# Kernel tuning notes

Measured on AMD Instinct MI355X. Metric: run time of the kernel, lower is better.

## Reference

```python
import jax, jax.numpy as jnp
import numpy as np

EPS = 1e-12  # torch F.normalize default eps (clamp_min)

def _l2norm(v, axis):
    n = jnp.sqrt(jnp.sum(v * v, axis=axis, keepdims=True))
    return v / jnp.maximum(n, EPS)

def setup_inputs() -> dict:
    key = jax.random.key(0)
    k1, k2, k3 = jax.random.split(key, 3)
    N, D, H, W, K = 64, 128, 64, 64, 32
    x = jax.random.normal(k1, (N, D, H, W), dtype=jnp.float32)
    conv_w = jax.random.normal(k2, (K, D), dtype=jnp.float32)  # 1x1 conv weight, no bias
    centroids = jax.random.uniform(k3, (K, D), dtype=jnp.float32)
    return {"x": x, "conv_w": conv_w, "centroids": centroids}

def reference(x, conv_w, centroids):
    N, D, H, W = x.shape
    K = conv_w.shape[0]
    # descriptor-wise L2 normalization over channel dim
    x = _l2norm(x, axis=1)
    xf = x.reshape(N, D, H * W)                      # [N, D, P]
    # 1x1 conv == per-pixel linear: [K,D] @ [N,D,P] -> [N,K,P]
    logits = jnp.einsum('kd,ndp->nkp', conv_w, xf)
    soft_assign = jax.nn.softmax(logits, axis=1)     # softmax over clusters
    # vlad[n,k,d] = sum_p a[n,k,p]*(x[n,d,p] - c[k,d])
    #            = (a @ x^T)[n,k,d] - (sum_p a)[n,k] * c[k,d]
    agg = jnp.einsum('nkp,ndp->nkd', soft_assign, xf)
    asum = jnp.sum(soft_assign, axis=2)              # [N, K]
    vlad = agg - asum[:, :, None] * centroids[None]  # [N, K, D]
    vlad = _l2norm(vlad, axis=2)                     # intra-normalization
    vlad = vlad.reshape(N, K * D)
    vlad = _l2norm(vlad, axis=1)                     # global L2 norm
    return vlad
```

## Files before the change

kernel.cpp:

```cpp
#include <hip/hip_runtime.h>
#include <math.h>

#define N_IMG 64
#define D_CH  128
#define P_PIX 4096
#define K_CL  32
#define S_SPL 8
#define P_BLK (P_PIX / S_SPL)
#define TP    32
#define N_TILE (P_BLK / TP)

typedef __attribute__((ext_vector_type(8))) short bf16x8;
typedef __attribute__((ext_vector_type(4))) float f32x4;

#define MFMA(a, b, c) __builtin_amdgcn_mfma_f32_16x16x32_bf16(a, b, c, 0, 0, 0)

#define BAR() do {                                            \
    asm volatile("s_waitcnt lgkmcnt(0)" ::: "memory");        \
    __builtin_amdgcn_s_barrier();                             \
} while (0)

static __device__ __forceinline__ void split4t(float a, float b, float c, float d,
                                               ushort4 &h, ushort4 &l) {
    unsigned ua = __float_as_uint(a), ub = __float_as_uint(b);
    unsigned uc = __float_as_uint(c), ud = __float_as_uint(d);
    h.x = (ushort)(ua >> 16); h.y = (ushort)(ub >> 16);
    h.z = (ushort)(uc >> 16); h.w = (ushort)(ud >> 16);
    float ra = a - __uint_as_float(ua & 0xffff0000u);
    float rb = b - __uint_as_float(ub & 0xffff0000u);
    float rc = c - __uint_as_float(uc & 0xffff0000u);
    float rd = d - __uint_as_float(ud & 0xffff0000u);
    l.x = (ushort)(__float_as_uint(ra) >> 16);
    l.y = (ushort)(__float_as_uint(rb) >> 16);
    l.z = (ushort)(__float_as_uint(rc) >> 16);
    l.w = (ushort)(__float_as_uint(rd) >> 16);
}

#define STAGE_AND_PREFETCH(tt) do {                                          \
    const int cc_ = (tt) & 1;                                                \
    _Pragma("unroll")                                                        \
    for (int it = 0; it < 4; ++it) {                                         \
        int d_ = it * 32 + (tid >> 3);                                       \
        ushort4 h_, lo_;                                                     \
        split4t(xv[it].x, xv[it].y, xv[it].z, xv[it].w, h_, lo_);            \
        *(ushort4*)&xDh[cc_][d_ * 40 + 4 * (tid & 7)] = h_;                  \
        *(ushort4*)&xDl[cc_][d_ * 40 + 4 * (tid & 7)] = lo_;                 \
    }                                                                        \
    float sq_ = 0.f;                                                         \
    _Pragma("unroll")                                                        \
    for (int c_ = 0; c_ < 4; ++c_) {                                         \
        ushort4 h_, lo_;                                                     \
        split4t(tv[4*c_+0], tv[4*c_+1], tv[4*c_+2], tv[4*c_+3], h_, lo_);    \
        *(ushort4*)&xTh[pT * 136 + dbase + 4 * c_] = h_;                     \
        *(ushort4*)&xTl[pT * 136 + dbase + 4 * c_] = lo_;                    \
        sq_ += tv[4*c_+0]*tv[4*c_+0] + tv[4*c_+1]*tv[4*c_+1]                 \
             + tv[4*c_+2]*tv[4*c_+2] + tv[4*c_+3]*tv[4*c_+3];                \
    }                                                                        \
    sq_ += __shfl_xor(sq_, 32);                                              \
    if (l < 32) pbuf[wid][pT] = sq_;                                         \
    if ((tt) + 1 < N_TILE) {                                                 \
        const float* xt2_ = xin + ((tt) + 1) * TP;                           \
        _Pragma("unroll")                                                    \
        for (int it = 0; it < 4; ++it) {                                     \
            int d_ = it * 32 + (tid >> 3);                                   \
            xv[it] = *(const float4*)(xt2_ + d_ * P_PIX + 4 * (tid & 7));    \
        }                                                                    \
        _Pragma("unroll")                                                    \
        for (int j_ = 0; j_ < 16; ++j_)                                      \
            tv[j_] = xt2_[(size_t)(dbase + j_) * P_PIX + pT];                \
    }                                                                        \
} while (0)

__global__ __launch_bounds__(256)
void netvlad_main(const float* __restrict__ x, const float* __restrict__ w,
                  float* __restrict__ aggp, float* __restrict__ asump)
{
    __shared__ __align__(16) ushort xTh[32 * 136], xTl[32 * 136];
    __shared__ __align__(16) ushort xDh[2][128 * 40], xDl[2][128 * 40];
    __shared__ __align__(16) ushort aph[2][32 * 40],  apl[2][32 * 40];
    __shared__ __align__(16) float  xch[4][64][4];
    __shared__ float pbuf[4][32];
    __shared__ float asw[4][16];

    const int tid = threadIdx.x;
    const int n   = blockIdx.x >> 3;
    const int ps  = blockIdx.x & 7;

    const int l   = tid & 63;
    const int wid = tid >> 6;
    const int q   = l >> 4;
    const int ln  = l & 15;
    const int mt  = wid >> 1;
    const int nt  = wid & 1;

    bf16x8 wh[4], wl[4];
    #pragma unroll
    for (int kk = 0; kk < 4; ++kk) {
        const float* wp = w + (nt * 16 + ln) * D_CH + kk * 32 + 8 * q;
        float4 wa = *(const float4*)wp;
        float4 wb = *(const float4*)(wp + 4);
        ushort4 h1, l1, h2, l2;
        split4t(wa.x, wa.y, wa.z, wa.w, h1, l1);
        split4t(wb.x, wb.y, wb.z, wb.w, h2, l2);
        wh[kk][0] = (short)h1.x; wh[kk][1] = (short)h1.y; wh[kk][2] = (short)h1.z; wh[kk][3] = (short)h1.w;
        wh[kk][4] = (short)h2.x; wh[kk][5] = (short)h2.y; wh[kk][6] = (short)h2.z; wh[kk][7] = (short)h2.w;
        wl[kk][0] = (short)l1.x; wl[kk][1] = (short)l1.y; wl[kk][2] = (short)l1.z; wl[kk][3] = (short)l1.w;
        wl[kk][4] = (short)l2.x; wl[kk][5] = (short)l2.y; wl[kk][6] = (short)l2.z; wl[kk][7] = (short)l2.w;
    }

    f32x4 acc2[2][2];
    #pragma unroll
    for (int a = 0; a < 2; ++a)
        #pragma unroll
        for (int b = 0; b < 2; ++b)
            acc2[a][b] = (f32x4){0.f, 0.f, 0.f, 0.f};
    float asacc = 0.0f;

    const float* xin = x + (size_t)n * D_CH * P_PIX + ps * P_BLK;

    const int pT    = tid & 31;
    const int dbase = (tid >> 5) * 16;

    float4 xv[4];
    float  tv[16];
    {
        const float* xt = xin;
        #pragma unroll
        for (int it = 0; it < 4; ++it) {
            int d = it * 32 + (tid >> 3);
            xv[it] = *(const float4*)(xt + d * P_PIX + 4 * (tid & 7));
        }
        #pragma unroll
        for (int j = 0; j < 16; ++j)
            tv[j] = xt[(size_t)(dbase + j) * P_PIX + pT];
    }
    STAGE_AND_PREFETCH(0);

    for (int t = 0; t < N_TILE; ++t) {
        const int c = t & 1;
        BAR();

        float spx, spy, spz, spw;
        {
            int pp = l & 31;
            int jb = (l >> 5) * 2;
            float vsq = pbuf[jb][pp] + pbuf[jb + 1][pp];
            vsq += __shfl_xor(vsq, 32);
            float sSl = 1.0f / fmaxf(sqrtf(vsq), 1e-12f);
            int p0 = mt * 16 + 4 * q;
            spx = __shfl(sSl, p0 + 0);
            spy = __shfl(sSl, p0 + 1);
            spz = __shfl(sSl, p0 + 2);
            spw = __shfl(sSl, p0 + 3);
        }

        f32x4 acc1 = (f32x4){0.f, 0.f, 0.f, 0.f};
        #pragma unroll
        for (int kk = 0; kk < 4; ++kk) {
            int ia = (mt * 16 + ln) * 136 + kk * 32 + 8 * q;
            bf16x8 Ah = *(const bf16x8*)&xTh[ia];
            bf16x8 Al = *(const bf16x8*)&xTl[ia];
            acc1 = MFMA(Ah, wh[kk], acc1);
            acc1 = MFMA(Ah, wl[kk], acc1);
            acc1 = MFMA(Al, wh[kk], acc1);
        }

        float e[4], s[4];
        e[0] = __builtin_expf(acc1[0] * spx);
        e[1] = __builtin_expf(acc1[1] * spy);
        e[2] = __builtin_expf(acc1[2] * spz);
        e[3] = __builtin_expf(acc1[3] * spw);
        #pragma unroll
        for (int r = 0; r < 4; ++r) {
            s[r] = e[r];
            s[r] += __shfl_xor(s[r], 1);
            s[r] += __shfl_xor(s[r], 2);
            s[r] += __shfl_xor(s[r], 4);
            s[r] += __shfl_xor(s[r], 8);
        }
        *(float4*)&xch[wid][l][0] = make_float4(s[0], s[1], s[2], s[3]);
        BAR();
        {
            float4 po = *(const float4*)&xch[wid ^ 1][l][0];
            float rt[4];
            rt[0] = __builtin_amdgcn_rcpf(s[0] + po.x);
            rt[1] = __builtin_amdgcn_rcpf(s[1] + po.y);
            rt[2] = __builtin_amdgcn_rcpf(s[2] + po.z);
            rt[3] = __builtin_amdgcn_rcpf(s[3] + po.w);
            float sm[4], ap[4];
            #pragma unroll
            for (int r = 0; r < 4; ++r) sm[r] = e[r] * rt[r];
            asacc += sm[0] + sm[1] + sm[2] + sm[3];
            ap[0] = sm[0] * spx; ap[1] = sm[1] * spy;
            ap[2] = sm[2] * spz; ap[3] = sm[3] * spw;
            ushort4 h, lo;
            split4t(ap[0], ap[1], ap[2], ap[3], h, lo);
            int ib = (nt * 16 + ln) * 40 + mt * 16 + 4 * q;
            *(ushort4*)&aph[c][ib] = h;
            *(ushort4*)&apl[c][ib] = lo;
        }
        BAR();

        bf16x8 A2h[2], A2l[2], B2h[2], B2l[2];
        #pragma unroll
        for (int m2 = 0; m2 < 2; ++m2) {
            int ia = ((2 * wid + m2) * 16 + ln) * 40 + 8 * q;
            A2h[m2] = *(const bf16x8*)&xDh[c][ia];
            A2l[m2] = *(const bf16x8*)&xDl[c][ia];
        }
        #pragma unroll
        for (int n2 = 0; n2 < 2; ++n2) {
            int ib = (n2 * 16 + ln) * 40 + 8 * q;
            B2h[n2] = *(const bf16x8*)&aph[c][ib];
            B2l[n2] = *(const bf16x8*)&apl[c][ib];
        }
        #pragma unroll
        for (int m2 = 0; m2 < 2; ++m2)
            #pragma unroll
            for (int n2 = 0; n2 < 2; ++n2) {
                acc2[m2][n2] = MFMA(A2h[m2], B2h[n2], acc2[m2][n2]);
                acc2[m2][n2] = MFMA(A2h[m2], B2l[n2], acc2[m2][n2]);
                acc2[m2][n2] = MFMA(A2l[m2], B2h[n2], acc2[m2][n2]);
            }
        if (t + 1 < N_TILE) {
            STAGE_AND_PREFETCH(t + 1);
        }
    }

    const int base = ((n * S_SPL + ps) * K_CL) * D_CH;
    #pragma unroll
    for (int m2 = 0; m2 < 2; ++m2)
        #pragma unroll
        for (int n2 = 0; n2 < 2; ++n2) {
            int k = n2 * 16 + ln;
            #pragma unroll
            for (int r = 0; r < 4; ++r) {
                int d = (2 * wid + m2) * 16 + 4 * q + r;
                aggp[base + k * D_CH + d] = acc2[m2][n2][r];
            }
        }
    asacc += __shfl_xor(asacc, 16);
    asacc += __shfl_xor(asacc, 32);
    if (l < 16) asw[wid][l] = asacc;
    __syncthreads();
    if (tid < K_CL)
        asump[(n * S_SPL + ps) * K_CL + tid] =
            asw[tid >> 4][tid & 15] + asw[(tid >> 4) + 2][tid & 15];
}

__global__ __launch_bounds__(256)
void netvlad_finish(const float* __restrict__ aggp, const float* __restrict__ asump,
                    const float* __restrict__ cen, float* __restrict__ out)
{
    __shared__ float red[K_CL][8];
    __shared__ float gw[4];
    __shared__ float gss;
    const int tid = threadIdx.x;
    const int n = blockIdx.x;
    const int k = tid >> 3;
    const int d0 = (tid & 7) << 4;

    float v[16];
    #pragma unroll
    for (int i = 0; i < 16; ++i) v[i] = 0.0f;
    float as = 0.0f;
    for (int qq = 0; qq < S_SPL; ++qq) {
        const float* src = aggp + (((n * S_SPL + qq) * K_CL) + k) * D_CH + d0;
        #pragma unroll
        for (int c = 0; c < 4; ++c) {
            float4 t4 = *(const float4*)(src + (c << 2));
            v[4*c+0] += t4.x; v[4*c+1] += t4.y; v[4*c+2] += t4.z; v[4*c+3] += t4.w;
        }
        as += asump[(n * S_SPL + qq) * K_CL + k];
    }
    const float* cp = cen + k * D_CH + d0;
    float ssq = 0.0f;
    #pragma unroll
    for (int c = 0; c < 4; ++c) {
        float4 c4 = *(const float4*)(cp + (c << 2));
        v[4*c+0] -= as * c4.x;
        v[4*c+1] -= as * c4.y;
        v[4*c+2] -= as * c4.z;
        v[4*c+3] -= as * c4.w;
    }
    #pragma unroll
    for (int i = 0; i < 16; ++i) ssq += v[i] * v[i];
    red[k][tid & 7] = ssq;
    __syncthreads();
    float s2 = 0.0f;
    #pragma unroll
    for (int j = 0; j < 8; ++j) s2 += red[k][j];
    const float sc1 = 1.0f / fmaxf(sqrtf(s2), 1e-12f);
    #pragma unroll
    for (int i = 0; i < 16; ++i) v[i] *= sc1;
    float g = ssq * sc1 * sc1;
    #pragma unroll
    for (int off = 1; off < 64; off <<= 1) g += __shfl_xor(g, off);
    if ((tid & 63) == 0) gw[tid >> 6] = g;
    __syncthreads();
    if (tid == 0) gss = 1.0f / fmaxf(sqrtf(gw[0] + gw[1] + gw[2] + gw[3]), 1e-12f);
    __syncthreads();
    const float gsc = gss;
    float* op = out + (size_t)n * (K_CL * D_CH) + k * D_CH + d0;
    #pragma unroll
    for (int c = 0; c < 4; ++c) {
        *(float4*)(op + (c << 2)) =
            make_float4(v[4*c+0]*gsc, v[4*c+1]*gsc, v[4*c+2]*gsc, v[4*c+3]*gsc);
    }
}

extern "C" void kernel_launch(void* const* d_in, const int* in_sizes, int n_in,
                              void* d_out, int out_size, void* d_ws, size_t ws_size,
                              hipStream_t stream)
{
    const float* x   = (const float*)d_in[0];
    const float* w   = (const float*)d_in[1];
    const float* cen = (const float*)d_in[2];
    float* out = (float*)d_out;

    float* aggp  = (float*)d_ws;
    float* asump = aggp + (size_t)N_IMG * S_SPL * K_CL * D_CH;

    netvlad_main<<<N_IMG * S_SPL, 256, 0, stream>>>(x, w, aggp, asump);
    netvlad_finish<<<N_IMG, 256, 0, stream>>>(aggp, asump, cen, out);
}
```

Measured before the change: 51.56 us.

## Fuse finish kernel into main via last-block-done atomic counter

Removes the separate finish kernel launch. Each main block increments a per-image counter after writing its partials, and the last of the 8 blocks for an image does the reduction, centroid subtraction and both L2 normalizations. This saves a kernel launch and the gap between kernels, but adds a hipMemsetAsync on the counters, thread fences, and a serialized tail inside the last block for each image.

```diff
diff --git a/kernel.cpp b/kernel.cpp
--- a/kernel.cpp
+++ b/kernel.cpp
@@ -73,7 +73,9 @@
 
 __global__ __launch_bounds__(256)
 void netvlad_main(const float* __restrict__ x, const float* __restrict__ w,
-                  float* __restrict__ aggp, float* __restrict__ asump)
+                  const float* __restrict__ cen, float* __restrict__ out,
+                  float* __restrict__ aggp, float* __restrict__ asump,
+                  int* __restrict__ cnt)
 {
     __shared__ __align__(16) ushort xTh[32 * 136], xTl[32 * 136];
     __shared__ __align__(16) ushort xDh[2][128 * 40], xDl[2][128 * 40];
@@ -81,6 +83,10 @@
     __shared__ __align__(16) float  xch[4][64][4];
     __shared__ float pbuf[4][32];
     __shared__ float asw[4][16];
+    __shared__ float fred[K_CL][8];
+    __shared__ float fgw[4];
+    __shared__ float fgss;
+    __shared__ int   ffin;
 
     const int tid = threadIdx.x;
     const int n   = blockIdx.x >> 3;
@@ -246,66 +252,66 @@
     if (tid < K_CL)
         asump[(n * S_SPL + ps) * K_CL + tid] =
             asw[tid >> 4][tid & 15] + asw[(tid >> 4) + 2][tid & 15];
-}
-
-__global__ __launch_bounds__(256)
-void netvlad_finish(const float* __restrict__ aggp, const float* __restrict__ asump,
-                    const float* __restrict__ cen, float* __restrict__ out)
-{
-    __shared__ float red[K_CL][8];
-    __shared__ float gw[4];
-    __shared__ float gss;
-    const int tid = threadIdx.x;
-    const int n = blockIdx.x;
-    const int k = tid >> 3;
-    const int d0 = (tid & 7) << 4;
-
-    float v[16];
-    #pragma unroll
-    for (int i = 0; i < 16; ++i) v[i] = 0.0f;
-    float as = 0.0f;
-    for (int qq = 0; qq < S_SPL; ++qq) {
-        const float* src = aggp + (((n * S_SPL + qq) * K_CL) + k) * D_CH + d0;
-        #pragma unroll
-        for (int c = 0; c < 4; ++c) {
-            float4 t4 = *(const float4*)(src + (c << 2));
-            v[4*c+0] += t4.x; v[4*c+1] += t4.y; v[4*c+2] += t4.z; v[4*c+3] += t4.w;
-        }
-        as += asump[(n * S_SPL + qq) * K_CL + k];
-    }
-    const float* cp = cen + k * D_CH + d0;
-    float ssq = 0.0f;
-    #pragma unroll
-    for (int c = 0; c < 4; ++c) {
-        float4 c4 = *(const float4*)(cp + (c << 2));
-        v[4*c+0] -= as * c4.x;
-        v[4*c+1] -= as * c4.y;
-        v[4*c+2] -= as * c4.z;
-        v[4*c+3] -= as * c4.w;
-    }
-    #pragma unroll
-    for (int i = 0; i < 16; ++i) ssq += v[i] * v[i];
-    red[k][tid & 7] = ssq;
+
+    __threadfence();
     __syncthreads();
-    float s2 = 0.0f;
-    #pragma unroll
-    for (int j = 0; j < 8; ++j) s2 += red[k][j];
-    const float sc1 = 1.0f / fmaxf(sqrtf(s2), 1e-12f);
-    #pragma unroll
-    for (int i = 0; i < 16; ++i) v[i] *= sc1;
-    float g = ssq * sc1 * sc1;
-    #pragma unroll
-    for (int off = 1; off < 64; off <<= 1) g += __shfl_xor(g, off);
-    if ((tid & 63) == 0) gw[tid >> 6] = g;
+    if (tid == 0) {
+        int prev = __atomic_fetch_add(cnt + n, 1, __ATOMIC_RELAXED);
+        ffin = (prev == S_SPL - 1);
+    }
     __syncthreads();
-    if (tid == 0) gss = 1.0f / fmaxf(sqrtf(gw[0] + gw[1] + gw[2] + gw[3]), 1e-12f);
-    __syncthreads();
-    const float gsc = gss;
-    float* op = out + (size_t)n * (K_CL * D_CH) + k * D_CH + d0;
-    #pragma unroll
-    for (int c = 0; c < 4; ++c) {
-        *(float4*)(op + (c << 2)) =
-            make_float4(v[4*c+0]*gsc, v[4*c+1]*gsc, v[4*c+2]*gsc, v[4*c+3]*gsc);
+    if (ffin) {
+        __threadfence();
+        const int kf = tid >> 3;
+        const int df = (tid & 7) << 4;
+
+        float v[16];
+        #pragma unroll
+        for (int i = 0; i < 16; ++i) v[i] = 0.0f;
+        float as = 0.0f;
+        for (int qq = 0; qq < S_SPL; ++qq) {
+            const float* src = aggp + (((n * S_SPL + qq) * K_CL) + kf) * D_CH + df;
+            #pragma unroll
+            for (int cb = 0; cb < 4; ++cb) {
+                float4 t4 = *(const float4*)(src + (cb << 2));
+                v[4*cb+0] += t4.x; v[4*cb+1] += t4.y; v[4*cb+2] += t4.z; v[4*cb+3] += t4.w;
+            }
+            as += asump[(n * S_SPL + qq) * K_CL + kf];
+        }
+        const float* cp = cen + kf * D_CH + df;
+        float ssq = 0.0f;
+        #pragma unroll
+        for (int cb = 0; cb < 4; ++cb) {
+            float4 c4 = *(const float4*)(cp + (cb << 2));
+            v[4*cb+0] -= as * c4.x;
+            v[4*cb+1] -= as * c4.y;
+            v[4*cb+2] -= as * c4.z;
+            v[4*cb+3] -= as * c4.w;
+        }
+        #pragma unroll
+        for (int i = 0; i < 16; ++i) ssq += v[i] * v[i];
+        fred[kf][tid & 7] = ssq;
+        __syncthreads();
+        float s2 = 0.0f;
+        #pragma unroll
+        for (int j = 0; j < 8; ++j) s2 += fred[kf][j];
+        const float sc1 = 1.0f / fmaxf(sqrtf(s2), 1e-12f);
+        #pragma unroll
+        for (int i = 0; i < 16; ++i) v[i] *= sc1;
+        float g = ssq * sc1 * sc1;
+        #pragma unroll
+        for (int off = 1; off < 64; off <<= 1) g += __shfl_xor(g, off);
+        if ((tid & 63) == 0) fgw[tid >> 6] = g;
+        __syncthreads();
+        if (tid == 0) fgss = 1.0f / fmaxf(sqrtf(fgw[0] + fgw[1] + fgw[2] + fgw[3]), 1e-12f);
+        __syncthreads();
+        const float gsc = fgss;
+        float* op = out + (size_t)n * (K_CL * D_CH) + kf * D_CH + df;
+        #pragma unroll
+        for (int cb = 0; cb < 4; ++cb) {
+            *(float4*)(op + (cb << 2)) =
+                make_float4(v[4*cb+0]*gsc, v[4*cb+1]*gsc, v[4*cb+2]*gsc, v[4*cb+3]*gsc);
+        }
     }
 }
 
@@ -320,7 +326,8 @@
 
     float* aggp  = (float*)d_ws;
     float* asump = aggp + (size_t)N_IMG * S_SPL * K_CL * D_CH;
-
-    netvlad_main<<<N_IMG * S_SPL, 256, 0, stream>>>(x, w, aggp, asump);
-    netvlad_finish<<<N_IMG, 256, 0, stream>>>(aggp, asump, cen, out);
+    int*   cnt   = (int*)(asump + (size_t)N_IMG * S_SPL * K_CL);
+
+    hipMemsetAsync(cnt, 0, N_IMG * sizeof(int), stream);
+    netvlad_main<<<N_IMG * S_SPL, 256, 0, stream>>>(x, w, cen, out, aggp, asump, cnt);
 }
```

Result: slower. 138.6 us (+168.7%).
